# Kernel optimization log

Hardware: AMD Instinct MI355X
Metric: run time of the kernel (lower is better)

Reference implementation:

```python
import jax, jax.numpy as jnp
import numpy as np
from jax import lax

DN = ('NCDHW', 'OIDHW', 'NCDHW')

def conv3d(x, w, b=None):
    y = lax.conv_general_dilated(x, w, window_strides=(1, 1, 1), padding='SAME', dimension_numbers=DN)
    if b is not None:
        y = y + b[None, :, None, None, None]
    return y

def adaptive_conv(x, w):
    # x: [B,C,D,H,W]; w: [B,27,D,H,W] per-voxel 3x3x3 kernel weights
    B, C, D, H, W = x.shape
    xp = jnp.pad(x, ((0, 0), (0, 0), (1, 1), (1, 1), (1, 1)))
    out = jnp.zeros_like(x)
    idx = 0
    for i in range(3):
        for j in range(3):
            for k in range(3):
                out = out + xp[:, :, i:i + D, j:j + H, k:k + W] * w[:, idx][:, None]
                idx += 1
    return out

def setup_inputs() -> dict:
    key = jax.random.key(0)
    k1, k2, k3 = jax.random.split(key, 3)
    B, C, D, H, W = 1, 8, 128, 128, 128
    x = jax.random.normal(k1, (B, C, D, H, W), dtype=jnp.float32)
    w1 = jax.random.normal(k2, (8, 8, 3, 3, 3), dtype=jnp.float32) * 0.1
    b1 = jnp.zeros((8,), dtype=jnp.float32)
    w2 = jax.random.normal(k3, (27, 8, 3, 3, 3), dtype=jnp.float32) * 0.1
    return {"x": x, "w1": w1, "b1": b1, "w2": w2}

def reference(x, w1, b1, w2):
    # adaptive_block: per-voxel 27-tap weights from a small conv stack
    h = jax.nn.relu(conv3d(x, w1, b1))
    w = conv3d(h, w2)  # [B,27,D,H,W]
    # F.normalize(w, dim=1, p=1)
    n = jnp.sum(jnp.abs(w), axis=1, keepdims=True)
    w = w / jnp.maximum(n, 1e-12)
    out = x
    for _ in range(3):
        out = adaptive_conv(out, w)
    return out
```

## Files before the change

### kernel.cpp

```cpp
#include <hip/hip_runtime.h>
#include <hip/hip_bf16.h>

constexpr int HW2 = 16384;
constexpr int DHW = 2097152;

constexpr int PKG = 13;
constexpr int XT  = 130;

typedef short bf16x8 __attribute__((ext_vector_type(8)));
typedef float f32x4  __attribute__((ext_vector_type(4)));

__device__ inline unsigned short f2b(float f) {
  __hip_bfloat16 h = __float2bfloat16(f);
  return *(unsigned short*)&h;
}
__device__ inline float b2f(unsigned short u) {
  __hip_bfloat16 h = *(__hip_bfloat16*)&u;
  return __bfloat162float(h);
}

__global__ __launch_bounds__(256) void k_prep(
    const float* __restrict__ w1, const float* __restrict__ w2,
    unsigned short* __restrict__ Wpack2, unsigned short* __restrict__ Wpack1,
    float* __restrict__ g_ti, float* __restrict__ g_xi) {
  int i = blockIdx.x * 256 + threadIdx.x;
  if (i < 9216) {
    int j = i & 7;
    int lane = (i >> 3) & 63;
    int Mt = (i >> 9) & 1;
    int g2 = i >> 10;
    int s = g2 % 3, dx = g2 / 3;
    int oc = Mt * 16 + (lane & 15);
    int kr = s * 32 + (lane >> 4) * 8 + j;
    int ci = kr & 7, g = kr >> 3;
    float w = 0.f;
    if (oc < 27 && g < 9) {
      int dzr = g / 3, dyr = g % 3;
      w = w2[(oc * 8 + ci) * 27 + dzr * 9 + dyr * 3 + dx];
    }
    Wpack2[i] = f2b(w);
  }
  int jj = i - 9216;
  if (jj >= 0 && jj < 4608) {
    int j = jj & 7;
    int lane = (jj >> 3) & 63;
    int g2 = jj >> 9;
    int s = g2 % 3, dx = g2 / 3;
    int oc = lane & 15;
    int kr = s * 32 + (lane >> 4) * 8 + j;
    int ci = kr & 7, g = kr >> 3;
    float w = 0.f;
    if (oc < 8 && g < 9) {
      int dzr = g / 3, dyr = g % 3;
      w = w1[(oc * 8 + ci) * 27 + dzr * 9 + dyr * 3 + dx];
    }
    Wpack1[jj] = f2b(w);
  }
  int gg = i - 13824;
  if (gg >= 0 && gg < 32) {
    float* p = (gg < 8)  ? (g_ti - 8 + gg)
             : (gg < 16) ? (g_ti + (size_t)8 * DHW + (gg - 8))
             : (gg < 24) ? (g_xi - 8 + (gg - 16))
                         : (g_xi + (size_t)8 * DHW + (gg - 24));
    *p = 0.f;
  }
}

__global__ __launch_bounds__(256) void k_xpose(
    const float* __restrict__ x, unsigned short* __restrict__ xb,
    float* __restrict__ xi) {
  int idx = blockIdx.x * 256 + threadIdx.x;
  float f[8];
  unsigned v[4];
#pragma unroll
  for (int p = 0; p < 4; ++p) {
    f[2 * p]     = x[(size_t)(2 * p) * DHW + idx];
    f[2 * p + 1] = x[(size_t)(2 * p + 1) * DHW + idx];
    unsigned lo = f2b(f[2 * p]);
    unsigned hi = f2b(f[2 * p + 1]);
    v[p] = lo | (hi << 16);
  }
  ((uint4*)xb)[idx] = make_uint4(v[0], v[1], v[2], v[3]);
  float4* xo = (float4*)(xi + (size_t)idx * 8);
  xo[0] = make_float4(f[0], f[1], f[2], f[3]);
  xo[1] = make_float4(f[4], f[5], f[6], f[7]);
}

__global__ __launch_bounds__(256) void k_conv1m(
    const unsigned short* __restrict__ xb,
    const unsigned short* __restrict__ Wpack1,
    const float* __restrict__ b1, unsigned short* __restrict__ hb) {
  __shared__ __align__(16) unsigned short T[XT * PKG * 8];
  const int tid  = threadIdx.x;
  const int lane = tid & 63;
  const int wv   = tid >> 6;
  const int z0 = blockIdx.x >> 7;
  const int y0 = blockIdx.x & 127;

  bf16x8 wf[3][3];
  {
    const bf16x8* wp = (const bf16x8*)Wpack1;
#pragma unroll
    for (int dx = 0; dx < 3; ++dx)
#pragma unroll
      for (int s = 0; s < 3; ++s)
        wf[dx][s] = wp[(dx * 3 + s) * 64 + lane];
  }

  const uint4* src = (const uint4*)xb;
  uint4* dst = (uint4*)T;
#pragma unroll 1
  for (int c = tid; c < 12 * XT; c += 256) {
    int g  = c / XT;
    int xi = c - g * XT;
    uint4 v = make_uint4(0u, 0u, 0u, 0u);
    if (g < 9) {
      int z = z0 + g / 3 - 1, y = y0 + g % 3 - 1, xg = xi - 1;
      if ((unsigned)z < 128u && (unsigned)y < 128u && (unsigned)xg < 128u)
        v = src[(z * 128 + y) * 128 + xg];
    }
    dst[xi * PKG + g] = v;
  }
  __syncthreads();

  f32x4 acc[2];
#pragma unroll
  for (int nt = 0; nt < 2; ++nt) acc[nt] = (f32x4){0.f, 0.f, 0.f, 0.f};

  const int n = lane & 15;
  const int q = lane >> 4;
  const int xbase = wv * 32 + n;

#pragma unroll
  for (int dx = 0; dx < 3; ++dx) {
#pragma unroll
    for (int s = 0; s < 3; ++s) {
      bf16x8 bfr[2];
#pragma unroll
      for (int nt = 0; nt < 2; ++nt) {
        int off = ((xbase + nt * 16 + dx) * PKG + (s * 4 + q)) * 8;
        bfr[nt] = *(const bf16x8*)&T[off];
      }
#pragma unroll
      for (int nt = 0; nt < 2; ++nt)
        acc[nt] = __builtin_amdgcn_mfma_f32_16x16x32_bf16(
            wf[dx][s], bfr[nt], acc[nt], 0, 0, 0);
    }
  }

  const int voxrow = (z0 * 128 + y0) * 128;
  if (q < 2) {
#pragma unroll
    for (int nt = 0; nt < 2; ++nt) {
      const int vox = voxrow + wv * 32 + nt * 16 + n;
      ushort4 o;
      o.x = f2b(fmaxf(acc[nt][0] + b1[q * 4 + 0], 0.f));
      o.y = f2b(fmaxf(acc[nt][1] + b1[q * 4 + 1], 0.f));
      o.z = f2b(fmaxf(acc[nt][2] + b1[q * 4 + 2], 0.f));
      o.w = f2b(fmaxf(acc[nt][3] + b1[q * 4 + 3], 0.f));
      *(ushort4*)(hb + (size_t)vox * 8 + q * 4) = o;
    }
  }
}

__global__ __launch_bounds__(256) void k_conv2(
    const unsigned short* __restrict__ hb,
    const unsigned short* __restrict__ Wpack2,
    unsigned short* __restrict__ wn) {
  __shared__ __align__(16) unsigned short T[XT * PKG * 8];
  const int tid  = threadIdx.x;
  const int lane = tid & 63;
  const int wv   = tid >> 6;
  const int z0 = blockIdx.x >> 7;
  const int y0 = blockIdx.x & 127;

  bf16x8 wf[3][3][2];
  {
    const bf16x8* wp = (const bf16x8*)Wpack2;
#pragma unroll
    for (int dx = 0; dx < 3; ++dx)
#pragma unroll
      for (int s = 0; s < 3; ++s)
#pragma unroll
        for (int mt = 0; mt < 2; ++mt)
          wf[dx][s][mt] = wp[((dx * 3 + s) * 2 + mt) * 64 + lane];
  }

  const uint4* src = (const uint4*)hb;
  uint4* dst = (uint4*)T;
#pragma unroll 1
  for (int c = tid; c < 12 * XT; c += 256) {
    int g  = c / XT;
    int xi = c - g * XT;
    uint4 v = make_uint4(0u, 0u, 0u, 0u);
    if (g < 9) {
      int z = z0 + g / 3 - 1, y = y0 + g % 3 - 1, xg = xi - 1;
      if ((unsigned)z < 128u && (unsigned)y < 128u && (unsigned)xg < 128u)
        v = src[(z * 128 + y) * 128 + xg];
    }
    dst[xi * PKG + g] = v;
  }
  __syncthreads();

  f32x4 acc[2][2];
#pragma unroll
  for (int nt = 0; nt < 2; ++nt)
#pragma unroll
    for (int mt = 0; mt < 2; ++mt) acc[nt][mt] = (f32x4){0.f, 0.f, 0.f, 0.f};

  const int n = lane & 15;
  const int q = lane >> 4;
  const int xbase = wv * 32 + n;

#pragma unroll
  for (int dx = 0; dx < 3; ++dx) {
#pragma unroll
    for (int s = 0; s < 3; ++s) {
      bf16x8 bfr[2];
#pragma unroll
      for (int nt = 0; nt < 2; ++nt) {
        int off = ((xbase + nt * 16 + dx) * PKG + (s * 4 + q)) * 8;
        bfr[nt] = *(const bf16x8*)&T[off];
      }
#pragma unroll
      for (int mt = 0; mt < 2; ++mt)
#pragma unroll
        for (int nt = 0; nt < 2; ++nt)
          acc[nt][mt] = __builtin_amdgcn_mfma_f32_16x16x32_bf16(
              wf[dx][s][mt], bfr[nt], acc[nt][mt], 0, 0, 0);
    }
  }

  const int voxrow = (z0 * 128 + y0) * 128;
#pragma unroll
  for (int nt = 0; nt < 2; ++nt) {
    float ns = 0.f;
#pragma unroll
    for (int r = 0; r < 4; ++r) ns += fabsf(acc[nt][0][r]);
#pragma unroll
    for (int r = 0; r < 4; ++r) {
      int oc = 16 + q * 4 + r;
      ns += (oc < 27) ? fabsf(acc[nt][1][r]) : 0.f;
    }
    ns += __shfl_xor(ns, 16);
    ns += __shfl_xor(ns, 32);
    float sc = 1.f / fmaxf(ns, 1e-12f);
    const int vox = voxrow + wv * 32 + nt * 16 + n;
#pragma unroll
    for (int r = 0; r < 4; ++r) {
      int oc = q * 4 + r;
      wn[(size_t)oc * DHW + vox] = f2b(acc[nt][0][r] * sc);
    }
#pragma unroll
    for (int r = 0; r < 4; ++r) {
      int oc = 16 + q * 4 + r;
      if (oc < 27)
        wn[(size_t)oc * DHW + vox] = f2b(acc[nt][1][r] * sc);
    }
  }
}

__device__ inline int swzb(int off) { return off ^ (((off >> 7) & 7) << 4); }

template <int FINAL>
__global__ __launch_bounds__(256, 2) void k_adapt4(
    const float* __restrict__ in, const unsigned short* __restrict__ wn,
    float* __restrict__ out) {
  __shared__ __align__(16) char S[16 * 4224];
  const int tid = threadIdx.x;
  const int ty = blockIdx.x & 63, tz = blockIdx.x >> 6;
  const int y0 = ty * 2, z0 = tz * 2;

  uint4 stg[16];
#pragma unroll
  for (int c = 0; c < 16; ++c) {
    const int zs = min(max(z0 - 1 + (c >> 2), 0), 127);
    const int ys = min(max(y0 - 1 + (c & 3), 0), 127);
    stg[c] = ((const uint4*)(in + (size_t)(zs * 128 + ys) * 1024))[tid];
  }
  {
    const int off = swzb(32 + tid * 16);
#pragma unroll
    for (int c = 0; c < 16; ++c)
      *(uint4*)(S + c * 4224 + off) = stg[c];
  }
  if (tid < 64) {
    const int row = tid >> 2, part = tid & 3;
    const int off = (part < 2) ? part * 16 : (4128 + (part - 2) * 16);
    *(uint4*)(S + row * 4224 + swzb(off)) = make_uint4(0u, 0u, 0u, 0u);
  }
  __syncthreads();

  const int wv = tid >> 6, lane = tid & 63;
  const int zl = wv >> 1, yl = wv & 1;
  const int zout = z0 + zl, yout = y0 + yl;
  const int xg = lane * 2;
  const int vox0 = (zout * 128 + yout) * 128 + xg;

  int soff[4][2];
#pragma unroll
  for (int p = 0; p < 4; ++p)
#pragma unroll
    for (int h = 0; h < 2; ++h)
      soff[p][h] = swzb((xg + p) * 32 + h * 16);

  f32x4 a0A = (f32x4){0.f, 0.f, 0.f, 0.f};
  f32x4 a0B = (f32x4){0.f, 0.f, 0.f, 0.f};
  f32x4 a1A = (f32x4){0.f, 0.f, 0.f, 0.f};
  f32x4 a1B = (f32x4){0.f, 0.f, 0.f, 0.f};

#pragma unroll
  for (int g = 0; g < 9; ++g) {
    const int dzp = g / 3, dyp = g % 3;
    const char* R = S + ((zl + dzp) * 4 + (yl + dyp)) * 4224;
    f32x4 W[4][2];
#pragma unroll
    for (int p = 0; p < 4; ++p)
#pragma unroll
      for (int h = 0; h < 2; ++h)
        W[p][h] = *(const f32x4*)(R + soff[p][h]);
    const bool val = ((unsigned)(zout + dzp - 1) < 128u) &
                     ((unsigned)(yout + dyp - 1) < 128u);
#pragma unroll
    for (int dxi = 0; dxi < 3; ++dxi) {
      const unsigned u =
          *(const unsigned*)(wn + (size_t)(g * 3 + dxi) * DHW + vox0);
      const float wl = val ? b2f((unsigned short)(u & 0xffffu)) : 0.f;
      const float wh = val ? b2f((unsigned short)(u >> 16)) : 0.f;
#pragma unroll
      for (int c = 0; c < 4; ++c) {
        a0A[c] = fmaf(W[dxi][0][c], wl, a0A[c]);
        a0B[c] = fmaf(W[dxi][1][c], wl, a0B[c]);
        a1A[c] = fmaf(W[dxi + 1][0][c], wh, a1A[c]);
        a1B[c] = fmaf(W[dxi + 1][1][c], wh, a1B[c]);
      }
    }
  }

  if (FINAL) {
#pragma unroll
    for (int c = 0; c < 4; ++c) {
      *(float2*)(out + (size_t)c * DHW + vox0) = make_float2(a0A[c], a1A[c]);
      *(float2*)(out + (size_t)(c + 4) * DHW + vox0) =
          make_float2(a0B[c], a1B[c]);
    }
  } else {
    f32x4* op = (f32x4*)(out + (size_t)vox0 * 8);
    op[0] = a0A;
    op[1] = a0B;
    op[2] = a1A;
    op[3] = a1B;
  }
}

extern "C" void kernel_launch(void* const* d_in, const int* in_sizes, int n_in,
                              void* d_out, int out_size, void* d_ws, size_t ws_size,
                              hipStream_t stream) {
  const float* x  = (const float*)d_in[0];
  const float* w1 = (const float*)d_in[1];
  const float* b1 = (const float*)d_in[2];
  const float* w2 = (const float*)d_in[3];
  float* out = (float*)d_out;

  char* ws = (char*)d_ws;
  unsigned short* xb = (unsigned short*)ws;
  unsigned short* hb = (unsigned short*)(ws + (size_t)8 * DHW * 2);
  float* ti = (float*)(ws + 256);
  unsigned short* wn = (unsigned short*)(ws + (size_t)16 * DHW * 2 + 4096);
  float* xi = (float*)(ws + (size_t)16 * DHW * 2 + 4096 +
                       (size_t)27 * DHW * 2 + 8192);
  unsigned short* Wpack2 =
      (unsigned short*)((char*)xi + (size_t)8 * DHW * 4 + 16384);
  unsigned short* Wpack1 = Wpack2 + 9216;

  dim3 blk(256);
  k_prep<<<55, blk, 0, stream>>>(w1, w2, Wpack2, Wpack1, ti, xi);
  k_xpose<<<DHW / 256, blk, 0, stream>>>(x, xb, xi);
  k_conv1m<<<128 * 128, blk, 0, stream>>>(xb, Wpack1, b1, hb);
  k_conv2<<<128 * 128, blk, 0, stream>>>(hb, Wpack2, wn);
  k_adapt4<0><<<64 * 64, blk, 0, stream>>>(xi, wn, ti);
  k_adapt4<0><<<64 * 64, blk, 0, stream>>>(ti, wn, xi);
  k_adapt4<1><<<64 * 64, blk, 0, stream>>>(xi, wn, out);
}
```

Measured before the change: 418.0 us.

## Restructure conv halo staging and remap blocks for XCD-local L2 reuse

Replaces the divide-based staging loop in both conv kernels with a fixed unrolled staging macro. Each thread issues six independent predicated loads before writing them to LDS, which increases memory-level parallelism. The k-groups are repacked on a 4-stride (dz<<2|dy) layout, with the weight packing updated to match. Block indices in the conv and adaptive kernels are remapped so consecutive blocks on the same XCD handle neighboring z/y rows, improving L2 reuse of halo rows. The risk is a mismatch between the new group layout and the packed weights or the MFMA fragment reads.

```diff
diff --git a/kernel.cpp b/kernel.cpp
--- a/kernel.cpp
+++ b/kernel.cpp
@@ -34,8 +34,8 @@
     int kr = s * 32 + (lane >> 4) * 8 + j;
     int ci = kr & 7, g = kr >> 3;
     float w = 0.f;
-    if (oc < 27 && g < 9) {
-      int dzr = g / 3, dyr = g % 3;
+    if (oc < 27 && (g & 3) < 3) {
+      int dzr = g >> 2, dyr = g & 3;
       w = w2[(oc * 8 + ci) * 27 + dzr * 9 + dyr * 3 + dx];
     }
     Wpack2[i] = f2b(w);
@@ -50,8 +50,8 @@
     int kr = s * 32 + (lane >> 4) * 8 + j;
     int ci = kr & 7, g = kr >> 3;
     float w = 0.f;
-    if (oc < 8 && g < 9) {
-      int dzr = g / 3, dyr = g % 3;
+    if (oc < 8 && (g & 3) < 3) {
+      int dzr = g >> 2, dyr = g & 3;
       w = w1[(oc * 8 + ci) * 27 + dzr * 9 + dyr * 3 + dx];
     }
     Wpack1[jj] = f2b(w);
@@ -85,6 +85,34 @@
   xo[0] = make_float4(f[0], f[1], f[2], f[3]);
   xo[1] = make_float4(f[4], f[5], f[6], f[7]);
 }
+
+#define STAGE_ROWS(srcp)                                                   \
+  {                                                                        \
+    if (tid < 24) {                                                        \
+      int gh = tid >> 1, xih = (tid & 1) ? 129 : 0;                        \
+      dst[xih * PKG + gh] = make_uint4(0u, 0u, 0u, 0u);                    \
+    }                                                                      \
+    const int gg = tid >> 7;                                               \
+    const int xi_ = (tid & 127) + 1;                                       \
+    const int xg_ = xi_ - 1;                                               \
+    uint4 sv[6];                                                           \
+    bool vld[6];                                                           \
+    _Pragma("unroll")                                                      \
+    for (int it = 0; it < 6; ++it) {                                       \
+      const int g = gg + it * 2;                                           \
+      const int dz = g >> 2, dy = g & 3;                                   \
+      const int z = z0 + dz - 1, y = y0 + dy - 1;                          \
+      vld[it] = (dy < 3) & ((unsigned)z < 128u) & ((unsigned)y < 128u);    \
+      const int zz = vld[it] ? z : z0, yy = vld[it] ? y : y0;              \
+      sv[it] = (srcp)[(zz * 128 + yy) * 128 + xg_];                        \
+    }                                                                      \
+    _Pragma("unroll")                                                      \
+    for (int it = 0; it < 6; ++it) {                                       \
+      const int g = gg + it * 2;                                           \
+      uint4 v = vld[it] ? sv[it] : make_uint4(0u, 0u, 0u, 0u);             \
+      dst[xi_ * PKG + g] = v;                                              \
+    }                                                                      \
+  }
 
 __global__ __launch_bounds__(256) void k_conv1m(
     const unsigned short* __restrict__ xb,
@@ -94,8 +122,9 @@
   const int tid  = threadIdx.x;
   const int lane = tid & 63;
   const int wv   = tid >> 6;
-  const int z0 = blockIdx.x >> 7;
-  const int y0 = blockIdx.x & 127;
+  const int logical = (blockIdx.x & 7) * 2048 + (blockIdx.x >> 3);
+  const int z0 = logical >> 7;
+  const int y0 = logical & 127;
 
   bf16x8 wf[3][3];
   {
@@ -109,18 +138,7 @@
 
   const uint4* src = (const uint4*)xb;
   uint4* dst = (uint4*)T;
-#pragma unroll 1
-  for (int c = tid; c < 12 * XT; c += 256) {
-    int g  = c / XT;
-    int xi = c - g * XT;
-    uint4 v = make_uint4(0u, 0u, 0u, 0u);
-    if (g < 9) {
-      int z = z0 + g / 3 - 1, y = y0 + g % 3 - 1, xg = xi - 1;
-      if ((unsigned)z < 128u && (unsigned)y < 128u && (unsigned)xg < 128u)
-        v = src[(z * 128 + y) * 128 + xg];
-    }
-    dst[xi * PKG + g] = v;
-  }
+  STAGE_ROWS(src);
   __syncthreads();
 
   f32x4 acc[2];
@@ -171,8 +189,9 @@
   const int tid  = threadIdx.x;
   const int lane = tid & 63;
   const int wv   = tid >> 6;
-  const int z0 = blockIdx.x >> 7;
-  const int y0 = blockIdx.x & 127;
+  const int logical = (blockIdx.x & 7) * 2048 + (blockIdx.x >> 3);
+  const int z0 = logical >> 7;
+  const int y0 = logical & 127;
 
   bf16x8 wf[3][3][2];
   {
@@ -188,18 +207,7 @@
 
   const uint4* src = (const uint4*)hb;
   uint4* dst = (uint4*)T;
-#pragma unroll 1
-  for (int c = tid; c < 12 * XT; c += 256) {
-    int g  = c / XT;
-    int xi = c - g * XT;
-    uint4 v = make_uint4(0u, 0u, 0u, 0u);
-    if (g < 9) {
-      int z = z0 + g / 3 - 1, y = y0 + g % 3 - 1, xg = xi - 1;
-      if ((unsigned)z < 128u && (unsigned)y < 128u && (unsigned)xg < 128u)
-        v = src[(z * 128 + y) * 128 + xg];
-    }
-    dst[xi * PKG + g] = v;
-  }
+  STAGE_ROWS(src);
   __syncthreads();
 
   f32x4 acc[2][2];
@@ -268,7 +276,8 @@
     float* __restrict__ out) {
   __shared__ __align__(16) char S[16 * 4224];
   const int tid = threadIdx.x;
-  const int ty = blockIdx.x & 63, tz = blockIdx.x >> 6;
+  const int logical = (blockIdx.x & 7) * 512 + (blockIdx.x >> 3);
+  const int ty = logical & 63, tz = logical >> 6;
   const int y0 = ty * 2, z0 = tz * 2;
 
   uint4 stg[16];
```

Result: faster. 388.4 us (-7.1%).
